# Performance work log

Measured on AMD Instinct MI355X. Metric: run time of the kernel, lower is better.

Reference implementation:

```python
import jax, jax.numpy as jnp
import numpy as np

DN = ('NHWC', 'HWIO', 'NHWC')

def conv(x, w, stride=1):
    return jax.lax.conv_general_dilated(x, w, (stride, stride), 'SAME', dimension_numbers=DN)

def up2(x):
    return jnp.repeat(jnp.repeat(x, 2, axis=1), 2, axis=2)

def nms(boxes, scores, max_output=100, iou_thresh=0.5):
    # greedy sequential NMS, fixed trip count, padded outputs
    NEG = jnp.float32(-1e30)
    area = (boxes[:, 2] - boxes[:, 0]) * (boxes[:, 3] - boxes[:, 1])  # [N]
    def step(sw, _):
        idx = jnp.argmax(sw)
        s = sw[idx]
        b = boxes[idx]
        valid = s > NEG * 0.5
        y1 = jnp.maximum(b[0], boxes[:, 0]); x1 = jnp.maximum(b[1], boxes[:, 1])
        y2 = jnp.minimum(b[2], boxes[:, 2]); x2 = jnp.minimum(b[3], boxes[:, 3])
        inter = jnp.maximum(y2 - y1, 0.0) * jnp.maximum(x2 - x1, 0.0)
        barea = (b[2] - b[0]) * (b[3] - b[1])
        iou = inter / (barea + area - inter + 1e-9)
        sw = jnp.where(iou > iou_thresh, NEG, sw)  # suppress (includes self)
        out_b = jnp.where(valid, b, jnp.zeros(4, boxes.dtype))
        out_s = jnp.where(valid, s, jnp.float32(0.0))
        return sw, (out_b, out_s)
    _, (sel_boxes, sel_scores) = jax.lax.scan(step, scores, None, length=max_output)
    return sel_boxes, sel_scores

def setup_inputs() -> dict:
    key = jax.random.key(0)
    ks = jax.random.split(key, 16)
    def w(k, shape):
        fan_in = shape[0] * shape[1] * shape[2]
        return jax.random.normal(k, shape, jnp.float32) * jnp.sqrt(2.0 / fan_in)
    return {
        'inputs': jax.random.normal(ks[0], (1, 512, 512, 3), jnp.float32),
        # backbone (resnet50-style channel widths, strides 2/4/8/16/32)
        'w_stem': w(ks[1], (7, 7, 3, 64)),
        'w_c2': w(ks[2], (3, 3, 64, 256)),
        'w_c3': w(ks[3], (3, 3, 256, 512)),
        'w_c4': w(ks[4], (3, 3, 512, 1024)),
        'w_c5': w(ks[5], (3, 3, 1024, 2048)),
        # FPN laterals + output convs (channels=256)
        'l3': w(ks[6], (1, 1, 512, 256)),
        'l4': w(ks[7], (1, 1, 1024, 256)),
        'l5': w(ks[8], (1, 1, 2048, 256)),
        'o3': w(ks[9], (3, 3, 256, 256)),
        'o4': w(ks[10], (3, 3, 256, 256)),
        'o5': w(ks[11], (3, 3, 256, 256)),
        # RPN: shared 3x3 + obj head (num_anchors=1) + bbox head (4*num_anchors)
        'w_rpn': w(ks[12], (3, 3, 256, 256)),
        'w_obj': w(ks[13], (1, 1, 256, 1)),
        'w_box': w(ks[14], (1, 1, 256, 4)),
    }

def reference(inputs, w_stem, w_c2, w_c3, w_c4, w_c5, l3, l4, l5, o3, o4, o5, w_rpn, w_obj, w_box):
    relu = jax.nn.relu
    # backbone
    s = relu(conv(inputs, w_stem, 2))   # 256x256x64
    c2 = relu(conv(s, w_c2, 2))         # 128x128x256
    c3 = relu(conv(c2, w_c3, 2))        # 64x64x512
    c4 = relu(conv(c3, w_c4, 2))        # 32x32x1024
    c5 = relu(conv(c4, w_c5, 2))        # 16x16x2048
    # FPN
    p5 = conv(c5, l5)
    p4 = conv(c4, l4) + up2(p5)
    p3 = conv(c3, l3) + up2(p4)
    p3, p4, p5 = conv(p3, o3), conv(p4, o4), conv(p5, o5)
    # RPN over all levels (bbox deltas computed per original but unused downstream)
    obj_logits = []
    for p in (p3, p4, p5):
        t = relu(conv(p, w_rpn))
        obj_logits.append(conv(t, w_obj))
        _ = conv(t, w_box)
    obj = obj_logits[0]  # [B, h, w, A]
    B, h, w_, A = obj.shape
    scores = jax.nn.sigmoid(obj).reshape(B, -1)  # [B, h*w*A]
    # anchor grid (fixed 0.1-sized boxes), faithful to TF meshgrid default 'xy' indexing
    yy = jnp.linspace(0.0, 1.0, h)
    xx = jnp.linspace(0.0, 1.0, w_)
    Y, X = jnp.meshgrid(yy, xx)  # shape [w, h]
    boxes = jnp.stack([Y - 0.05, X - 0.05, Y + 0.05, X + 0.05], axis=-1)
    boxes = jnp.clip(boxes, 0.0, 1.0).reshape(-1, 4)  # [w*h, 4]
    sel_boxes, sel_scores = nms(boxes, scores[0], max_output=100, iou_thresh=0.5)
    return sel_boxes, sel_scores
```

## Files before the change

### kernel.cpp

```cpp
#include <hip/hip_runtime.h>
#include <hip/hip_bf16.h>

typedef float f4 __attribute__((ext_vector_type(4)));
typedef short s8v __attribute__((ext_vector_type(8)));
typedef unsigned short us4 __attribute__((ext_vector_type(4)));
typedef unsigned short us8 __attribute__((ext_vector_type(8)));

#define AP 40

__global__ __launch_bounds__(256) void stem_kernel(
    const float* __restrict__ in, const float* __restrict__ w,
    float* __restrict__ out)
{
  __shared__ float in_lds[37 * 37 * 3];
  __shared__ float w_lds[7 * 7 * 3 * 64];
  const int tid = threadIdx.x;
  const int ty0 = (blockIdx.x >> 4) * 16;
  const int tx0 = (blockIdx.x & 15) * 16;

  for (int idx = tid; idx < 9408; idx += 256) w_lds[idx] = w[idx];
  for (int idx = tid; idx < 4107; idx += 256) {
    int ci = idx % 3;
    int rem = idx / 3;
    int ix = rem % 37, iy = rem / 37;
    int gy = ty0 * 2 - 2 + iy, gx = tx0 * 2 - 2 + ix;
    float v = 0.f;
    if ((unsigned)gy < 512u && (unsigned)gx < 512u)
      v = in[(gy * 512 + gx) * 3 + ci];
    in_lds[idx] = v;
  }
  __syncthreads();

  const int co = (tid & 15) * 4;
  const int py = tid >> 4;
  f4 acc[16];
#pragma unroll
  for (int px = 0; px < 16; ++px) acc[px] = (f4)0.f;

  for (int ky = 0; ky < 7; ++ky)
    for (int kx = 0; kx < 7; ++kx)
#pragma unroll
      for (int ci = 0; ci < 3; ++ci) {
        f4 wv = *(const f4*)&w_lds[(((ky * 7 + kx) * 3) + ci) * 64 + co];
        const float* ip = &in_lds[((2 * py + ky) * 37 + kx) * 3 + ci];
#pragma unroll
        for (int px = 0; px < 16; ++px) {
          float iv = ip[px * 6];
          acc[px] += iv * wv;
        }
      }

#pragma unroll
  for (int px = 0; px < 16; ++px) {
    int oy = ty0 + py, ox = tx0 + px;
    f4 o = acc[px];
#pragma unroll
    for (int c = 0; c < 4; ++c) o[c] = fmaxf(o[c], 0.f);
    *(f4*)&out[(oy * 256 + ox) * 64 + co] = o;
  }
}

__global__ __launch_bounds__(256) void wsplit_kernel(
    const float* __restrict__ w, unsigned short* __restrict__ wt,
    int C_in, int C_out, int taps)
{
  __shared__ float t[64][68];
  const int tid = threadIdx.x;
  const int tap = blockIdx.z;
  const int ci0 = blockIdx.x * 64;
  const int co0 = blockIdx.y * 64;
  const size_t lstride = (size_t)taps * C_in * C_out;

#pragma unroll
  for (int q = 0; q < 4; ++q) {
    int f = q * 256 + tid;
    int r = f >> 4, c = f & 15;
    f4 v = *(const f4*)&w[((size_t)(tap * C_in + ci0 + r)) * C_out + co0 + c * 4];
    *(f4*)&t[r][c * 4] = v;
  }
  __syncthreads();

#pragma unroll
  for (int q = 0; q < 4; ++q) {
    int f = q * 256 + tid;
    int r = f >> 4, c = f & 15;
    us4 h, m, l;
#pragma unroll
    for (int u = 0; u < 4; ++u) {
      float s = t[c * 4 + u][r];
      unsigned int ub = __float_as_uint(s);
      unsigned short hh = (unsigned short)(ub >> 16);
      float r1 = s - __uint_as_float((unsigned int)hh << 16);
      unsigned short mm = (unsigned short)(__float_as_uint(r1) >> 16);
      float r2 = r1 - __uint_as_float((unsigned int)mm << 16);
      unsigned short ll = (unsigned short)(__float_as_uint(r2) >> 16);
      h[u] = hh; m[u] = mm; l[u] = ll;
    }
    size_t base = ((size_t)tap * C_out + co0 + r) * C_in + ci0 + c * 4;
    *(us4*)&wt[base] = h;
    *(us4*)&wt[lstride + base] = m;
    *(us4*)&wt[2 * lstride + base] = l;
  }
}

__global__ __launch_bounds__(256, 2) void conv_mfma(
    const float* __restrict__ in, const unsigned short* __restrict__ wt,
    float* __restrict__ pout,
    int H_in, int W_in, int C_in, int wshift, int C_out,
    int stride, int pad, int ci_per_z, int npix, int relu)
{
  __shared__ __align__(16) unsigned short At[3][128][AP];
  __shared__ __align__(16) unsigned short Bt[3][128][AP];
  const int tid = threadIdx.x;
  const int pix_base = blockIdx.x * 128;
  const int co_base = blockIdx.y * 128;
  const int ci_z0 = blockIdx.z * ci_per_z;
  const int wmask = (1 << wshift) - 1;
  const size_t lstride = (size_t)9 * C_in * C_out;

  const int lane = tid & 63, wv = tid >> 6;
  const int pixhalf = (wv >> 1) * 64, cohalf = (wv & 1) * 64;
  const int fm = lane & 15, fq = lane >> 4;

  int a_pix[4], a_c4[4], a_ys[4], a_xs[4];
#pragma unroll
  for (int q = 0; q < 4; ++q) {
    int f = q * 256 + tid;
    a_pix[q] = f >> 3; a_c4[q] = f & 7;
    int p = pix_base + a_pix[q];
    a_ys[q] = (p >> wshift) * stride - pad;
    a_xs[q] = (p & wmask) * stride - pad;
  }
  int b_col[2], b_seg[2];
#pragma unroll
  for (int q = 0; q < 2; ++q) {
    int f = q * 256 + tid;
    b_col[q] = f >> 2; b_seg[q] = (f & 3) * 8;
  }

  f4 acc[4][4];
#pragma unroll
  for (int i = 0; i < 4; ++i)
#pragma unroll
    for (int j = 0; j < 4; ++j) acc[i][j] = (f4)0.f;

  for (int ky = 0; ky < 3; ++ky) {
    for (int kx = 0; kx < 3; ++kx) {
      const int tap = ky * 3 + kx;
      bool aval[4];
      const float* aptr[4];
#pragma unroll
      for (int q = 0; q < 4; ++q) {
        int iy = a_ys[q] + ky;
        int ix = a_xs[q] + kx;
        aval[q] = ((unsigned)iy < (unsigned)H_in) && ((unsigned)ix < (unsigned)W_in);
        aptr[q] = in + (size_t)(iy * W_in + ix) * C_in + a_c4[q] * 4;
      }
      const unsigned short* bbase =
          wt + (size_t)tap * C_out * C_in + (size_t)co_base * C_in;

      for (int ci = ci_z0; ci < ci_z0 + ci_per_z; ci += 32) {
        __syncthreads();
#pragma unroll
        for (int q = 0; q < 4; ++q) {
          f4 av = (f4)0.f;
          if (aval[q]) av = *(const f4*)(aptr[q] + ci);
          us4 h, m, l;
#pragma unroll
          for (int u = 0; u < 4; ++u) {
            float s = av[u];
            unsigned int ub = __float_as_uint(s);
            unsigned short hh = (unsigned short)(ub >> 16);
            float r1 = s - __uint_as_float((unsigned int)hh << 16);
            unsigned short mm = (unsigned short)(__float_as_uint(r1) >> 16);
            float r2 = r1 - __uint_as_float((unsigned int)mm << 16);
            unsigned short ll = (unsigned short)(__float_as_uint(r2) >> 16);
            h[u] = hh; m[u] = mm; l[u] = ll;
          }
          *(us4*)&At[0][a_pix[q]][a_c4[q] * 4] = h;
          *(us4*)&At[1][a_pix[q]][a_c4[q] * 4] = m;
          *(us4*)&At[2][a_pix[q]][a_c4[q] * 4] = l;
        }
#pragma unroll
        for (int L = 0; L < 3; ++L) {
#pragma unroll
          for (int q = 0; q < 2; ++q) {
            const unsigned short* src =
                bbase + L * lstride + (size_t)b_col[q] * C_in + ci + b_seg[q];
            *(us8*)&Bt[L][b_col[q]][b_seg[q]] = *(const us8*)src;
          }
        }
        __syncthreads();

        s8v Bh[4], Bm[4], Bl[4];
#pragma unroll
        for (int j = 0; j < 4; ++j) {
          Bh[j] = *(const s8v*)&Bt[0][cohalf + j * 16 + fm][fq * 8];
          Bm[j] = *(const s8v*)&Bt[1][cohalf + j * 16 + fm][fq * 8];
          Bl[j] = *(const s8v*)&Bt[2][cohalf + j * 16 + fm][fq * 8];
        }
        {
          s8v Ah[4];
#pragma unroll
          for (int i = 0; i < 4; ++i)
            Ah[i] = *(const s8v*)&At[0][pixhalf + i * 16 + fm][fq * 8];
#pragma unroll
          for (int i = 0; i < 4; ++i)
#pragma unroll
            for (int j = 0; j < 4; ++j) {
              acc[i][j] = __builtin_amdgcn_mfma_f32_16x16x32_bf16(Ah[i], Bh[j], acc[i][j], 0, 0, 0);
              acc[i][j] = __builtin_amdgcn_mfma_f32_16x16x32_bf16(Ah[i], Bm[j], acc[i][j], 0, 0, 0);
              acc[i][j] = __builtin_amdgcn_mfma_f32_16x16x32_bf16(Ah[i], Bl[j], acc[i][j], 0, 0, 0);
            }
        }
        {
          s8v Am[4];
#pragma unroll
          for (int i = 0; i < 4; ++i)
            Am[i] = *(const s8v*)&At[1][pixhalf + i * 16 + fm][fq * 8];
#pragma unroll
          for (int i = 0; i < 4; ++i)
#pragma unroll
            for (int j = 0; j < 4; ++j) {
              acc[i][j] = __builtin_amdgcn_mfma_f32_16x16x32_bf16(Am[i], Bh[j], acc[i][j], 0, 0, 0);
              acc[i][j] = __builtin_amdgcn_mfma_f32_16x16x32_bf16(Am[i], Bm[j], acc[i][j], 0, 0, 0);
            }
        }
        {
          s8v Al[4];
#pragma unroll
          for (int i = 0; i < 4; ++i)
            Al[i] = *(const s8v*)&At[2][pixhalf + i * 16 + fm][fq * 8];
#pragma unroll
          for (int i = 0; i < 4; ++i)
#pragma unroll
            for (int j = 0; j < 4; ++j)
              acc[i][j] = __builtin_amdgcn_mfma_f32_16x16x32_bf16(Al[i], Bh[j], acc[i][j], 0, 0, 0);
        }
      }
    }
  }

  float* dst = pout + (size_t)blockIdx.z * npix * C_out;
#pragma unroll
  for (int i = 0; i < 4; ++i) {
#pragma unroll
    for (int j = 0; j < 4; ++j) {
#pragma unroll
      for (int r = 0; r < 4; ++r) {
        int p = pix_base + pixhalf + i * 16 + fq * 4 + r;
        int co = co_base + cohalf + j * 16 + fm;
        float v = acc[i][j][r];
        if (relu) v = fmaxf(v, 0.f);
        dst[(size_t)p * C_out + co] = v;
      }
    }
  }
}

__global__ __launch_bounds__(256) void reduce_relu_kernel(
    const float* __restrict__ p, float* __restrict__ out, int n4, int Z, int relu)
{
  int idx = blockIdx.x * 256 + threadIdx.x;
  if (idx >= n4) return;
  const f4* pv = (const f4*)p;
  f4 s = pv[idx];
  for (int z = 1; z < Z; ++z) s += pv[(size_t)z * n4 + idx];
  if (relu) {
#pragma unroll
    for (int c = 0; c < 4; ++c) s[c] = fmaxf(s[c], 0.f);
  }
  ((f4*)out)[idx] = s;
}

__global__ __launch_bounds__(256) void gemm64(
    const float* __restrict__ in, const float* __restrict__ w,
    float* __restrict__ pout, int C_in, int C_out, int ci_per_z, int npix)
{
  __shared__ __align__(16) float As2[32][68];
  __shared__ __align__(16) float Bs[32][64];
  const int tid = threadIdx.x;
  const int pix_base = blockIdx.x * 64;
  const int co_base = blockIdx.y * 64;
  const int ci_z0 = blockIdx.z * ci_per_z;
  const int tx = tid & 15, ty = tid >> 4;

  int ga_pix[2], ga_c4[2];
#pragma unroll
  for (int q = 0; q < 2; ++q) {
    int f = q * 256 + tid;
    ga_pix[q] = f >> 3; ga_c4[q] = f & 7;
  }
  int gb_row[2], gb_c4[2];
#pragma unroll
  for (int q = 0; q < 2; ++q) {
    int f = q * 256 + tid;
    gb_row[q] = f >> 4; gb_c4[q] = f & 15;
  }

  f4 acc[4];
#pragma unroll
  for (int i = 0; i < 4; ++i) acc[i] = (f4)0.f;

  for (int ci = ci_z0; ci < ci_z0 + ci_per_z; ci += 32) {
    __syncthreads();
#pragma unroll
    for (int q = 0; q < 2; ++q) {
      f4 av = *(const f4*)&in[(size_t)(pix_base + ga_pix[q]) * C_in + ci + ga_c4[q] * 4];
#pragma unroll
      for (int u = 0; u < 4; ++u) As2[ga_c4[q] * 4 + u][ga_pix[q]] = av[u];
    }
#pragma unroll
    for (int q = 0; q < 2; ++q) {
      *(f4*)&Bs[gb_row[q]][gb_c4[q] * 4] =
          *(const f4*)&w[(size_t)(ci + gb_row[q]) * C_out + co_base + gb_c4[q] * 4];
    }
    __syncthreads();
#pragma unroll
    for (int kk = 0; kk < 32; ++kk) {
      f4 a = *(const f4*)&As2[kk][ty * 4];
      f4 b = *(const f4*)&Bs[kk][tx * 4];
#pragma unroll
      for (int i = 0; i < 4; ++i) acc[i] += a[i] * b;
    }
  }

  float* dst = pout + (size_t)blockIdx.z * npix * C_out;
#pragma unroll
  for (int i = 0; i < 4; ++i)
    *(f4*)&dst[(size_t)(pix_base + ty * 4 + i) * C_out + co_base + tx * 4] = acc[i];
}

__global__ __launch_bounds__(256) void reduce_up2_kernel(
    const float* __restrict__ p, const float* __restrict__ res,
    float* __restrict__ out, int n4, int Z, int wshift)
{
  int idx = blockIdx.x * 256 + threadIdx.x;
  if (idx >= n4) return;
  const f4* pv = (const f4*)p;
  f4 s = pv[idx];
  for (int z = 1; z < Z; ++z) s += pv[(size_t)z * n4 + idx];
  if (res) {
    int pix = idx >> 6, c4 = idx & 63;
    int oy = pix >> wshift, ox = pix & ((1 << wshift) - 1);
    int rp = ((oy >> 1) << (wshift - 1)) + (ox >> 1);
    s += ((const f4*)res)[rp * 64 + c4];
  }
  ((f4*)out)[idx] = s;
}

__global__ __launch_bounds__(256) void obj_sigmoid_kernel(
    const float* __restrict__ t, const float* __restrict__ wobj,
    float* __restrict__ scores)
{
  __shared__ float wl[256];
  const int tid = threadIdx.x;
  wl[tid] = wobj[tid];
  __syncthreads();
  const int pix = blockIdx.x * 64 + (tid >> 2);
  const int c0 = (tid & 3) * 64;
  float acc = 0.f;
#pragma unroll
  for (int k = 0; k < 16; ++k) {
    f4 tv = *(const f4*)&t[(size_t)pix * 256 + c0 + k * 4];
    const float* wp = &wl[c0 + k * 4];
    acc += tv[0] * wp[0] + tv[1] * wp[1] + tv[2] * wp[2] + tv[3] * wp[3];
  }
  acc += __shfl_xor(acc, 1);
  acc += __shfl_xor(acc, 2);
  if ((tid & 3) == 0) scores[pix] = 1.f / (1.f + expf(-acc));
}

__global__ __launch_bounds__(1024) void nms_kernel(
    const float* __restrict__ scores, float* __restrict__ out)
{
  __shared__ unsigned long long keys[4096];
  __shared__ float acc_lds[100 * 8];
  const int tid = threadIdx.x;
  const float inv63 = 1.0f / 63.0f;

  if (tid < 125) ((f4*)out)[tid] = (f4)0.f;

#pragma unroll
  for (int r = 0; r < 4; ++r) {
    int idx = r * 1024 + tid;
    unsigned int bits = __float_as_uint(scores[idx]);
    keys[idx] = ((unsigned long long)(0x40000000u - bits) << 16) |
                (unsigned long long)idx;
  }

  int prev_cross = 1;
  for (int k = 2; k <= 4096; k <<= 1) {
    for (int j = k >> 1; j > 0; j >>= 1) {
      const int cross = (j > 32);
      if (cross | prev_cross) {
        __syncthreads();
      } else {
        asm volatile("s_waitcnt lgkmcnt(0)" ::: "memory");
      }
#pragma unroll
      for (int q = 0; q < 2; ++q) {
        int p = q * 1024 + tid;
        int i = ((p & ~(j - 1)) << 1) | (p & (j - 1));
        int partner = i | j;
        bool up = ((i & k) == 0);
        unsigned long long a = keys[i], b = keys[partner];
        if ((a > b) == up) { keys[i] = b; keys[partner] = a; }
      }
      prev_cross = cross;
    }
  }
  __syncthreads();

  if (tid >= 64) return;
  const int lane = tid;

  int n = 0;
  for (int b = 0; b < 64 && n < 100; ++b) {
    unsigned long long kk = keys[b * 64 + lane];
    int idx = (int)(kk & 0xFFFF);
    float sc = __uint_as_float(0x40000000u - (unsigned int)(kk >> 16));
    int si = idx >> 6, sj = idx & 63;
    float y = sj * inv63, x = si * inv63;
    float c0 = fmaxf(y - 0.05f, 0.f), c1 = fmaxf(x - 0.05f, 0.f);
    float c2 = fminf(y + 0.05f, 1.f), c3 = fminf(x + 0.05f, 1.f);
    float carea = (c2 - c0) * (c3 - c1);

    bool sup = false;
    for (int a = 0; a < n; ++a) {
      f4 ab = *(const f4*)&acc_lds[a * 8];
      float aarea = acc_lds[a * 8 + 4];
      float yy1 = fmaxf(ab[0], c0), xx1 = fmaxf(ab[1], c1);
      float yy2 = fminf(ab[2], c2), xx2 = fminf(ab[3], c3);
      float inter = fmaxf(yy2 - yy1, 0.f) * fmaxf(xx2 - xx1, 0.f);
      float iou = inter / (aarea + carea - inter + 1e-9f);
      sup = sup || (iou > 0.5f);
    }

    unsigned long long m = __ballot(!sup);
    while (m != 0 && n < 100) {
      int u = __builtin_ctzll(m);
      float b0 = __shfl(c0, u), b1 = __shfl(c1, u);
      float b2 = __shfl(c2, u), b3 = __shfl(c3, u);
      float ba = __shfl(carea, u);
      if (lane == u) {
        acc_lds[n * 8 + 0] = c0; acc_lds[n * 8 + 1] = c1;
        acc_lds[n * 8 + 2] = c2; acc_lds[n * 8 + 3] = c3;
        acc_lds[n * 8 + 4] = carea;
        out[n * 4 + 0] = c0; out[n * 4 + 1] = c1;
        out[n * 4 + 2] = c2; out[n * 4 + 3] = c3;
        out[400 + n] = sc;
        sup = true;
      }
      n++;
      if (lane > u && !sup) {
        float yy1 = fmaxf(b0, c0), xx1 = fmaxf(b1, c1);
        float yy2 = fminf(b2, c2), xx2 = fminf(b3, c3);
        float inter = fmaxf(yy2 - yy1, 0.f) * fmaxf(xx2 - xx1, 0.f);
        float iou = inter / (ba + carea - inter + 1e-9f);
        if (iou > 0.5f) sup = true;
      }
      m = __ballot(!sup);
    }
    __threadfence_block();
  }
}

extern "C" void kernel_launch(void* const* d_in, const int* in_sizes, int n_in,
                              void* d_out, int out_size, void* d_ws, size_t ws_size,
                              hipStream_t stream) {
  const float* x      = (const float*)d_in[0];
  const float* w_stem = (const float*)d_in[1];
  const float* w_c2   = (const float*)d_in[2];
  const float* w_c3   = (const float*)d_in[3];
  const float* w_c4   = (const float*)d_in[4];
  const float* w_c5   = (const float*)d_in[5];
  const float* l3     = (const float*)d_in[6];
  const float* l4     = (const float*)d_in[7];
  const float* l5     = (const float*)d_in[8];
  const float* o3w    = (const float*)d_in[9];
  const float* w_rpn  = (const float*)d_in[12];
  const float* w_obj  = (const float*)d_in[13];
  float* out = (float*)d_out;
  float* ws = (float*)d_ws;

  float* S   = ws;
  float* C2  = S   + 4194304;
  float* C3  = C2  + 4194304;
  float* C4  = C3  + 2097152;
  float* C5  = C4  + 1048576;
  float* P5  = C5  + 524288;
  float* P4  = P5  + 65536;
  float* P3P = P4  + 262144;
  float* P3  = P3P + 1048576;
  float* T   = P3  + 1048576;
  float* SC  = T   + 1048576;
  unsigned short* WT = (unsigned short*)(SC + 4096);
  float* PZ = (float*)(WT + 31457280);

  stem_kernel<<<256, 256, 0, stream>>>(x, w_stem, S);

  wsplit_kernel<<<dim3(1, 4, 9), 256, 0, stream>>>(w_c2, WT, 64, 256, 9);
  conv_mfma<<<dim3(128, 2, 2), 256, 0, stream>>>(
      S, WT, PZ, 256, 256, 64, 7, 256, 2, 0, 32, 16384, 0);
  reduce_relu_kernel<<<4096, 256, 0, stream>>>(PZ, C2, 1048576, 2, 1);

  wsplit_kernel<<<dim3(4, 8, 9), 256, 0, stream>>>(w_c3, WT, 256, 512, 9);
  conv_mfma<<<dim3(32, 4, 4), 256, 0, stream>>>(
      C2, WT, PZ, 128, 128, 256, 6, 512, 2, 0, 64, 4096, 0);
  reduce_relu_kernel<<<2048, 256, 0, stream>>>(PZ, C3, 524288, 4, 1);

  wsplit_kernel<<<dim3(8, 16, 9), 256, 0, stream>>>(w_c4, WT, 512, 1024, 9);
  conv_mfma<<<dim3(8, 8, 8), 256, 0, stream>>>(
      C3, WT, S, 64, 64, 512, 5, 1024, 2, 0, 64, 1024, 0);
  reduce_relu_kernel<<<1024, 256, 0, stream>>>(S, C4, 262144, 8, 1);

  wsplit_kernel<<<dim3(16, 32, 9), 256, 0, stream>>>(w_c5, WT, 1024, 2048, 9);
  conv_mfma<<<dim3(2, 16, 16), 256, 0, stream>>>(
      C4, WT, S, 32, 32, 1024, 4, 2048, 2, 0, 64, 256, 0);
  reduce_relu_kernel<<<512, 256, 0, stream>>>(S, C5, 131072, 16, 1);

  gemm64<<<dim3(4, 4, 8), 256, 0, stream>>>(C5, l5, S, 2048, 256, 256, 256);
  reduce_up2_kernel<<<64, 256, 0, stream>>>(S, nullptr, P5, 16384, 8, 4);
  gemm64<<<dim3(16, 4, 4), 256, 0, stream>>>(C4, l4, S, 1024, 256, 256, 1024);
  reduce_up2_kernel<<<256, 256, 0, stream>>>(S, P5, P4, 65536, 4, 5);
  gemm64<<<dim3(64, 4, 2), 256, 0, stream>>>(C3, l3, S, 512, 256, 256, 4096);
  reduce_up2_kernel<<<1024, 256, 0, stream>>>(S, P4, P3P, 262144, 2, 6);

  wsplit_kernel<<<dim3(4, 4, 9), 256, 0, stream>>>(o3w, WT, 256, 256, 9);
  conv_mfma<<<dim3(32, 2, 8), 256, 0, stream>>>(
      P3P, WT, S, 64, 64, 256, 6, 256, 1, 1, 32, 4096, 0);
  reduce_relu_kernel<<<1024, 256, 0, stream>>>(S, P3, 262144, 8, 0);

  wsplit_kernel<<<dim3(4, 4, 9), 256, 0, stream>>>(w_rpn, WT, 256, 256, 9);
  conv_mfma<<<dim3(32, 2, 8), 256, 0, stream>>>(
      P3, WT, S, 64, 64, 256, 6, 256, 1, 1, 32, 4096, 0);
  reduce_relu_kernel<<<1024, 256, 0, stream>>>(S, T, 262144, 8, 1);

  obj_sigmoid_kernel<<<64, 256, 0, stream>>>(T, w_obj, SC);
  nms_kernel<<<1, 1024, 0, stream>>>(SC, out);
}
```

Before: 702.5 us.

## Prefetch next conv chunk into registers and remap workgroups across XCDs

The conv_mfma main loop is flattened into a single chunk loop over taps and channel slices. Global loads for the next chunk are issued into registers right after the LDS barrier, and the fp32-to-3xbf16 split runs after the MFMA block. This is meant to hide global memory latency behind the MFMA work instead of stalling at the start of each iteration. Workgroup IDs are also remapped so that consecutive tiles share an XCD, which should improve L2 reuse. The costs are extra registers for the prefetch buffers and a chunk index decode that assumes the channel-slice count is a power of two with a particular shift, which only holds for small slice counts.

```diff
diff --git a/kernel.cpp b/kernel.cpp
--- a/kernel.cpp
+++ b/kernel.cpp
@@ -112,9 +112,18 @@
   __shared__ __align__(16) unsigned short At[3][128][AP];
   __shared__ __align__(16) unsigned short Bt[3][128][AP];
   const int tid = threadIdx.x;
-  const int pix_base = blockIdx.x * 128;
-  const int co_base = blockIdx.y * 128;
-  const int ci_z0 = blockIdx.z * ci_per_z;
+
+  const int nwg = gridDim.x * gridDim.y * gridDim.z;
+  const int hwid = blockIdx.x + gridDim.x * (blockIdx.y + gridDim.y * blockIdx.z);
+  const int wid = ((nwg & 7) == 0) ? (hwid & 7) * (nwg >> 3) + (hwid >> 3) : hwid;
+  const int bx = wid % gridDim.x;
+  const int brem = wid / gridDim.x;
+  const int by = brem % gridDim.y;
+  const int bz = brem / gridDim.y;
+
+  const int pix_base = bx * 128;
+  const int co_base = by * 128;
+  const int ci_z0 = bz * ci_per_z;
   const int wmask = (1 << wshift) - 1;
   const size_t lstride = (size_t)9 * C_in * C_out;
 
@@ -138,110 +147,131 @@
     b_col[q] = f >> 2; b_seg[q] = (f & 3) * 8;
   }
 
+  const int nc = ci_per_z >> 5;
+  const int ncsh = nc >> 1;
+  const int nchunks = 9 * nc;
+
+  f4 areg[4];
+  us8 breg[6];
+  auto issue_loads = [&](int c) {
+    int tap = c >> ncsh;
+    int ci = ci_z0 + (c & (nc - 1)) * 32;
+    int ky = tap / 3, kx = tap - ky * 3;
+#pragma unroll
+    for (int q = 0; q < 4; ++q) {
+      int iy = a_ys[q] + ky, ix = a_xs[q] + kx;
+      bool v = ((unsigned)iy < (unsigned)H_in) & ((unsigned)ix < (unsigned)W_in);
+      const float* p = in + (size_t)(iy * W_in + ix) * C_in + ci + a_c4[q] * 4;
+      areg[q] = v ? *(const f4*)p : (f4)0.f;
+    }
+    const unsigned short* bb =
+        wt + (size_t)tap * C_out * C_in + (size_t)co_base * C_in + ci;
+#pragma unroll
+    for (int L = 0; L < 3; ++L)
+#pragma unroll
+      for (int q = 0; q < 2; ++q)
+        breg[L * 2 + q] = *(const us8*)(bb + (size_t)L * lstride +
+                                        (size_t)b_col[q] * C_in + b_seg[q]);
+  };
+
+  us4 ah[4], am[4], al[4];
+  auto convert = [&]() {
+#pragma unroll
+    for (int q = 0; q < 4; ++q) {
+      f4 s4 = areg[q];
+      us4 h, m, l;
+#pragma unroll
+      for (int u = 0; u < 4; ++u) {
+        float s = s4[u];
+        unsigned int ub = __float_as_uint(s);
+        unsigned short hh = (unsigned short)(ub >> 16);
+        float r1 = s - __uint_as_float((unsigned int)hh << 16);
+        unsigned short mm = (unsigned short)(__float_as_uint(r1) >> 16);
+        float r2 = r1 - __uint_as_float((unsigned int)mm << 16);
+        unsigned short ll = (unsigned short)(__float_as_uint(r2) >> 16);
+        h[u] = hh; m[u] = mm; l[u] = ll;
+      }
+      ah[q] = h; am[q] = m; al[q] = l;
+    }
+  };
+
   f4 acc[4][4];
 #pragma unroll
   for (int i = 0; i < 4; ++i)
 #pragma unroll
     for (int j = 0; j < 4; ++j) acc[i][j] = (f4)0.f;
 
-  for (int ky = 0; ky < 3; ++ky) {
-    for (int kx = 0; kx < 3; ++kx) {
-      const int tap = ky * 3 + kx;
-      bool aval[4];
-      const float* aptr[4];
-#pragma unroll
-      for (int q = 0; q < 4; ++q) {
-        int iy = a_ys[q] + ky;
-        int ix = a_xs[q] + kx;
-        aval[q] = ((unsigned)iy < (unsigned)H_in) && ((unsigned)ix < (unsigned)W_in);
-        aptr[q] = in + (size_t)(iy * W_in + ix) * C_in + a_c4[q] * 4;
-      }
-      const unsigned short* bbase =
-          wt + (size_t)tap * C_out * C_in + (size_t)co_base * C_in;
-
-      for (int ci = ci_z0; ci < ci_z0 + ci_per_z; ci += 32) {
-        __syncthreads();
-#pragma unroll
-        for (int q = 0; q < 4; ++q) {
-          f4 av = (f4)0.f;
-          if (aval[q]) av = *(const f4*)(aptr[q] + ci);
-          us4 h, m, l;
-#pragma unroll
-          for (int u = 0; u < 4; ++u) {
-            float s = av[u];
-            unsigned int ub = __float_as_uint(s);
-            unsigned short hh = (unsigned short)(ub >> 16);
-            float r1 = s - __uint_as_float((unsigned int)hh << 16);
-            unsigned short mm = (unsigned short)(__float_as_uint(r1) >> 16);
-            float r2 = r1 - __uint_as_float((unsigned int)mm << 16);
-            unsigned short ll = (unsigned short)(__float_as_uint(r2) >> 16);
-            h[u] = hh; m[u] = mm; l[u] = ll;
-          }
-          *(us4*)&At[0][a_pix[q]][a_c4[q] * 4] = h;
-          *(us4*)&At[1][a_pix[q]][a_c4[q] * 4] = m;
-          *(us4*)&At[2][a_pix[q]][a_c4[q] * 4] = l;
+  issue_loads(0);
+  convert();
+
+  for (int c = 0; c < nchunks; ++c) {
+    __syncthreads();
+#pragma unroll
+    for (int q = 0; q < 4; ++q) {
+      *(us4*)&At[0][a_pix[q]][a_c4[q] * 4] = ah[q];
+      *(us4*)&At[1][a_pix[q]][a_c4[q] * 4] = am[q];
+      *(us4*)&At[2][a_pix[q]][a_c4[q] * 4] = al[q];
+    }
+#pragma unroll
+    for (int L = 0; L < 3; ++L)
+#pragma unroll
+      for (int q = 0; q < 2; ++q)
+        *(us8*)&Bt[L][b_col[q]][b_seg[q]] = breg[L * 2 + q];
+    __syncthreads();
+
+    const bool more = (c + 1 < nchunks);
+    if (more) issue_loads(c + 1);
+
+    s8v Bh[4], Bm[4], Bl[4];
+#pragma unroll
+    for (int j = 0; j < 4; ++j) {
+      Bh[j] = *(const s8v*)&Bt[0][cohalf + j * 16 + fm][fq * 8];
+      Bm[j] = *(const s8v*)&Bt[1][cohalf + j * 16 + fm][fq * 8];
+      Bl[j] = *(const s8v*)&Bt[2][cohalf + j * 16 + fm][fq * 8];
+    }
+    {
+      s8v Ah[4];
+#pragma unroll
+      for (int i = 0; i < 4; ++i)
+        Ah[i] = *(const s8v*)&At[0][pixhalf + i * 16 + fm][fq * 8];
+#pragma unroll
+      for (int i = 0; i < 4; ++i)
+#pragma unroll
+        for (int j = 0; j < 4; ++j) {
+          acc[i][j] = __builtin_amdgcn_mfma_f32_16x16x32_bf16(Ah[i], Bh[j], acc[i][j], 0, 0, 0);
+          acc[i][j] = __builtin_amdgcn_mfma_f32_16x16x32_bf16(Ah[i], Bm[j], acc[i][j], 0, 0, 0);
+          acc[i][j] = __builtin_amdgcn_mfma_f32_16x16x32_bf16(Ah[i], Bl[j], acc[i][j], 0, 0, 0);
         }
-#pragma unroll
-        for (int L = 0; L < 3; ++L) {
-#pragma unroll
-          for (int q = 0; q < 2; ++q) {
-            const unsigned short* src =
-                bbase + L * lstride + (size_t)b_col[q] * C_in + ci + b_seg[q];
-            *(us8*)&Bt[L][b_col[q]][b_seg[q]] = *(const us8*)src;
-          }
+    }
+    {
+      s8v Am[4];
+#pragma unroll
+      for (int i = 0; i < 4; ++i)
+        Am[i] = *(const s8v*)&At[1][pixhalf + i * 16 + fm][fq * 8];
+#pragma unroll
+      for (int i = 0; i < 4; ++i)
+#pragma unroll
+        for (int j = 0; j < 4; ++j) {
+          acc[i][j] = __builtin_amdgcn_mfma_f32_16x16x32_bf16(Am[i], Bh[j], acc[i][j], 0, 0, 0);
+          acc[i][j] = __builtin_amdgcn_mfma_f32_16x16x32_bf16(Am[i], Bm[j], acc[i][j], 0, 0, 0);
         }
-        __syncthreads();
-
-        s8v Bh[4], Bm[4], Bl[4];
-#pragma unroll
-        for (int j = 0; j < 4; ++j) {
-          Bh[j] = *(const s8v*)&Bt[0][cohalf + j * 16 + fm][fq * 8];
-          Bm[j] = *(const s8v*)&Bt[1][cohalf + j * 16 + fm][fq * 8];
-          Bl[j] = *(const s8v*)&Bt[2][cohalf + j * 16 + fm][fq * 8];
-        }
-        {
-          s8v Ah[4];
-#pragma unroll
-          for (int i = 0; i < 4; ++i)
-            Ah[i] = *(const s8v*)&At[0][pixhalf + i * 16 + fm][fq * 8];
-#pragma unroll
-          for (int i = 0; i < 4; ++i)
-#pragma unroll
-            for (int j = 0; j < 4; ++j) {
-              acc[i][j] = __builtin_amdgcn_mfma_f32_16x16x32_bf16(Ah[i], Bh[j], acc[i][j], 0, 0, 0);
-              acc[i][j] = __builtin_amdgcn_mfma_f32_16x16x32_bf16(Ah[i], Bm[j], acc[i][j], 0, 0, 0);
-              acc[i][j] = __builtin_amdgcn_mfma_f32_16x16x32_bf16(Ah[i], Bl[j], acc[i][j], 0, 0, 0);
-            }
-        }
-        {
-          s8v Am[4];
-#pragma unroll
-          for (int i = 0; i < 4; ++i)
-            Am[i] = *(const s8v*)&At[1][pixhalf + i * 16 + fm][fq * 8];
-#pragma unroll
-          for (int i = 0; i < 4; ++i)
-#pragma unroll
-            for (int j = 0; j < 4; ++j) {
-              acc[i][j] = __builtin_amdgcn_mfma_f32_16x16x32_bf16(Am[i], Bh[j], acc[i][j], 0, 0, 0);
-              acc[i][j] = __builtin_amdgcn_mfma_f32_16x16x32_bf16(Am[i], Bm[j], acc[i][j], 0, 0, 0);
-            }
-        }
-        {
-          s8v Al[4];
-#pragma unroll
-          for (int i = 0; i < 4; ++i)
-            Al[i] = *(const s8v*)&At[2][pixhalf + i * 16 + fm][fq * 8];
-#pragma unroll
-          for (int i = 0; i < 4; ++i)
-#pragma unroll
-            for (int j = 0; j < 4; ++j)
-              acc[i][j] = __builtin_amdgcn_mfma_f32_16x16x32_bf16(Al[i], Bh[j], acc[i][j], 0, 0, 0);
-        }
-      }
-    }
-  }
-
-  float* dst = pout + (size_t)blockIdx.z * npix * C_out;
+    }
+    {
+      s8v Al[4];
+#pragma unroll
+      for (int i = 0; i < 4; ++i)
+        Al[i] = *(const s8v*)&At[2][pixhalf + i * 16 + fm][fq * 8];
+#pragma unroll
+      for (int i = 0; i < 4; ++i)
+#pragma unroll
+        for (int j = 0; j < 4; ++j)
+          acc[i][j] = __builtin_amdgcn_mfma_f32_16x16x32_bf16(Al[i], Bh[j], acc[i][j], 0, 0, 0);
+    }
+
+    if (more) convert();
+  }
+
+  float* dst = pout + (size_t)bz * npix * C_out;
 #pragma unroll
   for (int i = 0; i < 4; ++i) {
 #pragma unroll
```

New measurement: 640.6 us. 1.1x faster.
